# Optimization experiments

Hardware: AMD Instinct MI355X
Metric: run time of the kernel (lower is better)

## Reference

```python
import jax, jax.numpy as jnp
import numpy as np

B, S, H = 2, 2048, 2560
NH, NKV, D = 8, 4, 256
SW = 1024
EPS = 1e-6
NEG = -1e9


def _rms(x, w=None, eps=EPS):
    y = x * jax.lax.rsqrt(jnp.mean(x * x, axis=-1, keepdims=True) + eps)
    return y * (1.0 + w) if w is not None else y


def _rope(x, cos, sin):
    # x: [B, h, S, D]; cos/sin: [1, 1, S, D] with duplicated half-frequencies
    half = x.shape[-1] // 2
    out = x * cos
    o1 = out[..., :half] - x[..., half:] * sin[..., :half]
    o2 = out[..., half:] + x[..., :half] * sin[..., half:]
    return jnp.concatenate([o1, o2], axis=-1)


def setup_inputs() -> dict:
    key = jax.random.key(0)
    ks = jax.random.split(key, 6)
    hidden_states = jax.random.normal(ks[0], (B, S, H), dtype=jnp.float32)
    Wq = jax.random.normal(ks[1], (NH * D, H), dtype=jnp.float32) * 0.02
    Wk = jax.random.normal(ks[2], (NKV * D, H), dtype=jnp.float32) * 0.02
    Wv = jax.random.normal(ks[3], (NKV * D, H), dtype=jnp.float32) * 0.02
    Wo = jax.random.normal(ks[4], (H, NH * D), dtype=jnp.float32) * 0.02
    q_norm_w = jnp.zeros((D,), dtype=jnp.float32)
    k_norm_w = jnp.zeros((D,), dtype=jnp.float32)
    # RoPE tables (standard theta=10000, duplicated halves as in torch ref)
    pos = jnp.arange(S, dtype=jnp.float32)
    inv = 1.0 / (10000.0 ** (jnp.arange(0, D, 2, dtype=jnp.float32) / D))
    freqs = pos[:, None] * inv[None, :]            # [S, D/2]
    emb = jnp.concatenate([freqs, freqs], axis=-1)  # [S, D]
    cos = jnp.cos(emb)[None, None]                 # [1,1,S,D]
    sin = jnp.sin(emb)[None, None]
    # causal + sliding-window additive mask (allowed: i-SW < j <= i)
    i = jnp.arange(S)[:, None]
    j = jnp.arange(S)[None, :]
    allowed = (j <= i) & (j > i - SW)
    attention_mask = jnp.where(allowed, 0.0, NEG).astype(jnp.float32)[None, None]
    return {"hidden_states": hidden_states, "attention_mask": attention_mask,
            "cos": cos, "sin": sin, "Wq": Wq, "Wk": Wk, "Wv": Wv, "Wo": Wo,
            "q_norm_w": q_norm_w, "k_norm_w": k_norm_w}


def reference(hidden_states, attention_mask, cos, sin, Wq, Wk, Wv, Wo, q_norm_w, k_norm_w):
    b, s, _ = hidden_states.shape
    xq = (hidden_states @ Wq.T).reshape(b, s, NH, D).transpose(0, 2, 1, 3)  # [B,NH,S,D]
    xq = _rms(xq, q_norm_w)
    xk = (hidden_states @ Wk.T).reshape(b, s, NKV, D)
    xv = (hidden_states @ Wv.T).reshape(b, s, NKV, D)
    xk = _rms(xk, k_norm_w)
    xv = _rms(xv)  # parameterless rms_norm on v
    xk = xk.transpose(0, 2, 1, 3)  # [B,NKV,S,D]
    xv = xv.transpose(0, 2, 1, 3)
    xq = _rope(xq, cos, sin)
    xk = _rope(xk, cos, sin)
    # expand_kv path: S >= sliding_window and NH != NKV -> repeat_interleave
    g = NH // NKV
    xk = jnp.repeat(xk, g, axis=1)
    xv = jnp.repeat(xv, g, axis=1)
    # scale=1.0 in original (no 1/sqrt(d))
    scores = jnp.einsum('bhqd,bhkd->bhqk', xq, xk) + attention_mask
    attn = jax.nn.softmax(scores, axis=-1)
    out = jnp.einsum('bhqk,bhkd->bhqd', attn, xv)
    out = out.transpose(0, 2, 1, 3).reshape(b, s, NH * D)
    return out @ Wo.T
```

## Files before the change

kernel.cpp:

```cpp
#include <hip/hip_runtime.h>

#define B_   2
#define S_   2048
#define H_   2560
#define NH_  8
#define NKV_ 4
#define D_   256
#define SW_  1024

#define QKV_LD 4096

typedef __attribute__((ext_vector_type(8))) short    short8;
typedef __attribute__((ext_vector_type(8))) _Float16 half8;
typedef __attribute__((ext_vector_type(4))) _Float16 half4;
typedef __attribute__((ext_vector_type(4))) float    floatx4;
typedef __attribute__((ext_vector_type(2))) float    floatx2;

typedef unsigned int __attribute__((address_space(1))) as1_uint;
typedef unsigned int __attribute__((address_space(3))) as3_uint;

static __device__ __forceinline__ void async16(const void* g, void* l) {
    __builtin_amdgcn_global_load_lds((const as1_uint*)g, (as3_uint*)l, 16, 0, 0);
}

__global__ __launch_bounds__(256) void conv_all(
    const float* __restrict__ s0, const float* __restrict__ s1,
    const float* __restrict__ s2, const float* __restrict__ s3,
    const float* __restrict__ s4,
    _Float16* __restrict__ d0, _Float16* __restrict__ d1,
    _Float16* __restrict__ d2, _Float16* __restrict__ d3,
    _Float16* __restrict__ d4)
{
    const float* src; _Float16* dst; int n4;
    switch (blockIdx.y) {
        case 0:  src = s0; dst = d0; n4 = 4096 * 2560 / 4; break;
        case 1:  src = s1; dst = d1; n4 = 2048 * 2560 / 4; break;
        case 2:  src = s2; dst = d2; n4 = 1024 * 2560 / 4; break;
        case 3:  src = s3; dst = d3; n4 = 1024 * 2560 / 4; break;
        default: src = s4; dst = d4; n4 = 2560 * 2048 / 4; break;
    }
    for (int i = blockIdx.x * 256 + threadIdx.x; i < n4; i += gridDim.x * 256) {
        floatx4 v = *(const floatx4*)(src + (size_t)i * 4);
        half4 h = { (_Float16)v.x, (_Float16)v.y, (_Float16)v.z, (_Float16)v.w };
        *(half4*)(dst + (size_t)i * 4) = h;
    }
}

template <int C_FP32>
__global__ __launch_bounds__(512, 2) void gemm256(
    const _Float16* __restrict__ A,
    const _Float16* __restrict__ Bm,
    void* __restrict__ Cv,
    int M, int N, int K, int NBX)
{
    (void)M;
    __shared__ __align__(16) _Float16 As[2][256 * 64];
    __shared__ __align__(16) _Float16 Bs[2][256 * 64];

    const int tid  = threadIdx.x;
    const int lane = tid & 63, w = tid >> 6;
    const int wr = w >> 2, wc = w & 3;
    const int quad = lane >> 4, l16 = lane & 15;

    const int nwg = gridDim.x, cpx = nwg >> 3;
    const int swz = (blockIdx.x & 7) * cpx + (blockIdx.x >> 3);
    const int mBase = (swz / NBX) * 256, nBase = (swz % NBX) * 256;

    const int NT = K >> 6;

    const int stRow = w * 8 + (lane >> 3);
    const int stCol = (((lane & 7) ^ (lane >> 3)) << 3);
    const int rdsw  = (l16 & 7) << 3;

    const _Float16* Ag = A  + (size_t)mBase * K;
    const _Float16* Bg = Bm + (size_t)nBase * K;

    floatx4 acc[8][4];
    const floatx4 fz = {0.f, 0.f, 0.f, 0.f};
#pragma unroll
    for (int i = 0; i < 8; ++i)
#pragma unroll
        for (int j = 0; j < 4; ++j) acc[i][j] = fz;

    auto stA = [&](int tt, int h, _Float16* dst) {
#pragma unroll
        for (int r = 0; r < 2; ++r) {
            const int rb = h * 128 + r * 64;
            async16(Ag + (size_t)(rb + stRow) * K + tt * 64 + stCol,
                    dst + (size_t)(rb + w * 8) * 64);
        }
    };
    auto stB = [&](int tt, int h, _Float16* dst) {
#pragma unroll
        for (int r = 0; r < 2; ++r) {
            const int rb = h * 128 + r * 64;
            async16(Bg + (size_t)(rb + stRow) * K + tt * 64 + stCol,
                    dst + (size_t)(rb + w * 8) * 64);
        }
    };

    stA(0, 0, &As[0][0]); stA(0, 1, &As[0][0]);
    stB(0, 0, &Bs[0][0]); stB(0, 1, &Bs[0][0]);
    if (NT > 1) { stB(1, 0, &Bs[1][0]); stB(1, 1, &Bs[1][0]); }
    asm volatile("s_waitcnt vmcnt(4)" ::: "memory");
    __builtin_amdgcn_s_barrier();

    auto tile = [&](int t, _Float16* Ab, _Float16* Bb, _Float16* Ao) {
        half8 bf[4][2], af[2][2];
#pragma unroll
        for (int c = 0; c < 4; ++c) {
            const int brow = wc * 64 + c * 16 + l16;
#pragma unroll
            for (int s = 0; s < 2; ++s)
                bf[c][s] = *(const half8*)&Bb[(size_t)brow * 64 + ((s * 32 + quad * 8) ^ rdsw)];
        }
#pragma unroll
        for (int r = 0; r < 2; ++r) {
            const int arow = wr * 128 + r * 16 + l16;
#pragma unroll
            for (int s = 0; s < 2; ++s)
                af[r][s] = *(const half8*)&Ab[(size_t)arow * 64 + ((s * 32 + quad * 8) ^ rdsw)];
        }
        if (t + 1 < NT) stA(t + 1, 0, Ao);
        asm volatile("s_waitcnt lgkmcnt(8)");
        __builtin_amdgcn_s_barrier();
        asm volatile("s_waitcnt lgkmcnt(0)");
        __builtin_amdgcn_s_setprio(1);
#pragma unroll
        for (int s = 0; s < 2; ++s)
#pragma unroll
            for (int c = 0; c < 4; ++c) {
                acc[0][c] = __builtin_amdgcn_mfma_f32_16x16x32_f16(af[0][s], bf[c][s], acc[0][c], 0, 0, 0);
                acc[1][c] = __builtin_amdgcn_mfma_f32_16x16x32_f16(af[1][s], bf[c][s], acc[1][c], 0, 0, 0);
            }
        __builtin_amdgcn_s_setprio(0);
        __builtin_amdgcn_s_barrier();
#pragma unroll
        for (int p = 1; p < 4; ++p) {
#pragma unroll
            for (int r = 0; r < 2; ++r) {
                const int arow = wr * 128 + (2 * p + r) * 16 + l16;
#pragma unroll
                for (int s = 0; s < 2; ++s)
                    af[r][s] = *(const half8*)&Ab[(size_t)arow * 64 + ((s * 32 + quad * 8) ^ rdsw)];
            }
            if (p == 1)      { if (t + 1 < NT) stA(t + 1, 1, Ao); }
            else if (p == 2) { if (t + 2 < NT) stB(t + 2, 0, Bb); }
            else             { if (t + 2 < NT) stB(t + 2, 1, Bb); }
            __builtin_amdgcn_s_barrier();
            asm volatile("s_waitcnt lgkmcnt(0)");
            __builtin_amdgcn_s_setprio(1);
#pragma unroll
            for (int s = 0; s < 2; ++s)
#pragma unroll
                for (int c = 0; c < 4; ++c) {
                    acc[2 * p][c]     = __builtin_amdgcn_mfma_f32_16x16x32_f16(af[0][s], bf[c][s], acc[2 * p][c], 0, 0, 0);
                    acc[2 * p + 1][c] = __builtin_amdgcn_mfma_f32_16x16x32_f16(af[1][s], bf[c][s], acc[2 * p + 1][c], 0, 0, 0);
                }
            __builtin_amdgcn_s_setprio(0);
            if (p == 3) {
                if (t < NT - 2) asm volatile("s_waitcnt vmcnt(4)" ::: "memory");
                else            asm volatile("s_waitcnt vmcnt(0)" ::: "memory");
            }
            __builtin_amdgcn_s_barrier();
        }
    };

    for (int t = 0; t < NT; t += 2) {
        tile(t,     &As[0][0], &Bs[0][0], &As[1][0]);
        tile(t + 1, &As[1][0], &Bs[1][0], &As[0][0]);
    }

#pragma unroll
    for (int fr = 0; fr < 8; ++fr) {
        const int row0 = mBase + wr * 128 + fr * 16 + quad * 4;
#pragma unroll
        for (int c = 0; c < 4; ++c) {
            const int col = nBase + wc * 64 + c * 16 + l16;
#pragma unroll
            for (int r = 0; r < 4; ++r) {
                const size_t idx = (size_t)(row0 + r) * N + col;
                if (C_FP32) ((float*)Cv)[idx] = acc[fr][c][r];
                else        ((_Float16*)Cv)[idx] = (_Float16)acc[fr][c][r];
            }
        }
    }
}

__global__ __launch_bounds__(256) void rmsrope_inplace(
    _Float16* __restrict__ qkv,
    const float* __restrict__ cosT,
    const float* __restrict__ sinT,
    const float* __restrict__ qw,
    const float* __restrict__ kw)
{
    const int t = blockIdx.x;
    const int s = t & (S_ - 1);
    const int tid = threadIdx.x, lane = tid & 63, w = tid >> 6;
    _Float16* row = qkv + (size_t)t * QKV_LD;
    const int d0 = lane * 2, d1 = 128 + lane * 2;

    floatx2 c0 = *(const floatx2*)(cosT + (size_t)s * D_ + d0);
    floatx2 c1 = *(const floatx2*)(cosT + (size_t)s * D_ + d1);
    floatx2 s0 = *(const floatx2*)(sinT + (size_t)s * D_ + d0);
    floatx2 s1 = *(const floatx2*)(sinT + (size_t)s * D_ + d1);
    floatx2 qw0 = *(const floatx2*)(qw + d0), qw1 = *(const floatx2*)(qw + d1);
    floatx2 kw0 = *(const floatx2*)(kw + d0), kw1 = *(const floatx2*)(kw + d1);

#pragma unroll
    for (int p = 0; p < 4; ++p) {
        const int v = w + p * 4;
        _Float16* x = row + v * D_;
        float x0a = (float)x[d0], x0b = (float)x[d0 + 1];
        float x1a = (float)x[d1], x1b = (float)x[d1 + 1];
        float ss = x0a * x0a + x0b * x0b + x1a * x1a + x1b * x1b;
#pragma unroll
        for (int off = 32; off > 0; off >>= 1) ss += __shfl_xor(ss, off, 64);
        const float rinv = rsqrtf(ss * (1.0f / 256.0f) + 1e-6f);
        if (v < 8) {
            const float y0a = x0a * rinv * (1.f + qw0.x), y0b = x0b * rinv * (1.f + qw0.y);
            const float y1a = x1a * rinv * (1.f + qw1.x), y1b = x1b * rinv * (1.f + qw1.y);
            x[d0] = (_Float16)(y0a * c0.x - y1a * s0.x);
            x[d0 + 1] = (_Float16)(y0b * c0.y - y1b * s0.y);
            x[d1] = (_Float16)(y1a * c1.x + y0a * s1.x);
            x[d1 + 1] = (_Float16)(y1b * c1.y + y0b * s1.y);
        } else if (v < 12) {
            const float y0a = x0a * rinv * (1.f + kw0.x), y0b = x0b * rinv * (1.f + kw0.y);
            const float y1a = x1a * rinv * (1.f + kw1.x), y1b = x1b * rinv * (1.f + kw1.y);
            x[d0] = (_Float16)(y0a * c0.x - y1a * s0.x);
            x[d0 + 1] = (_Float16)(y0b * c0.y - y1b * s0.y);
            x[d1] = (_Float16)(y1a * c1.x + y0a * s1.x);
            x[d1 + 1] = (_Float16)(y1b * c1.y + y0b * s1.y);
        } else {
            x[d0] = (_Float16)(x0a * rinv);
            x[d0 + 1] = (_Float16)(x0b * rinv);
            x[d1] = (_Float16)(x1a * rinv);
            x[d1 + 1] = (_Float16)(x1b * rinv);
        }
    }
}

__global__ __launch_bounds__(256) void transpose_v(
    const _Float16* __restrict__ qkv, _Float16* __restrict__ Vt)
{
    __shared__ _Float16 tile[64][66];
    const int s0 = blockIdx.x * 64;
    const int dd0 = blockIdx.y * 64;
    const int bk = blockIdx.z;
    const int b = bk >> 2, kvh = bk & 3;
    const _Float16* src = qkv + (size_t)(b * S_) * QKV_LD + 3072 + kvh * D_;
    _Float16* dst = Vt + (size_t)bk * D_ * S_;
    const int tx = threadIdx.x & 63, ty = threadIdx.x >> 6;
    for (int r = ty; r < 64; r += 4)
        tile[r][tx] = src[(size_t)(s0 + r) * QKV_LD + dd0 + tx];
    __syncthreads();
    for (int r = ty; r < 64; r += 4)
        dst[(size_t)(dd0 + r) * S_ + s0 + tx] = tile[tx][r];
}

#define PS_STRIDE 40

__global__ __launch_bounds__(256, 2) void attn_kernel(
    const _Float16* __restrict__ qkv,
    const _Float16* __restrict__ Vt,
    _Float16* __restrict__ Oa)
{
    __shared__ __align__(16) _Float16 Ks[2][32 * 256];
    __shared__ __align__(16) _Float16 Vs[2][256 * 32];
    __shared__ __align__(16) _Float16 Ps[4][16 * PS_STRIDE];

    const int idx = blockIdx.x;
    const int swz = (idx & 7) * 64 + (idx >> 3);
    const int qt = swz & 31, h = (swz >> 5) & 7, b = swz >> 8;
    const int qb = qt * 64;
    const int kvh = h >> 1;

    const int tid = threadIdx.x, lane = tid & 63, w = tid >> 6;
    const int quad = lane >> 4, l16 = lane & 15;
    const int q0 = qb + w * 16;

    const _Float16* Qrow = qkv + ((size_t)(b * S_ + q0 + l16)) * QKV_LD + h * D_;
    half8 qf[8];
#pragma unroll
    for (int kst = 0; kst < 8; ++kst)
        qf[kst] = *(const half8*)(Qrow + kst * 32 + quad * 8);

    floatx4 o[16];
    const floatx4 fzero = {0.f, 0.f, 0.f, 0.f};
#pragma unroll
    for (int dt = 0; dt < 16; ++dt) o[dt] = fzero;
    float mrow[4] = {-50000.f, -50000.f, -50000.f, -50000.f};
    float lrow[4] = {0.f, 0.f, 0.f, 0.f};

    const _Float16* Kbase  = qkv + (size_t)(b * S_) * QKV_LD + 2048 + kvh * D_;
    const _Float16* Vtbase = Vt + (size_t)(b * NKV_ + kvh) * D_ * S_;
    const int kb_start = (qb >= SW_) ? qb - SW_ : 0;
    const int kb_end = qb + 32;

    auto stage = [&](int kb, int bufi) {
#pragma unroll
        for (int p = 0; p < 4; ++p) {
            const int keyl = w * 8 + p * 2 + (lane >> 5);
            const int g = ((lane & 31) - keyl) & 31;
            async16(Kbase + (size_t)(kb + keyl) * QKV_LD + g * 8,
                    &Ks[bufi][(w * 8 + p * 2) * 256]);
        }
#pragma unroll
        for (int p = 0; p < 4; ++p) {
            const int drow = w * 64 + p * 16 + (lane >> 2);
            const int q = lane & 3;
            async16(Vtbase + (size_t)drow * S_ + kb + q * 8,
                    &Vs[bufi][(w * 64 + p * 16) * 32]);
        }
    };

    int buf = 0;
    stage(kb_start, 0);

    for (int kb = kb_start; kb <= kb_end; kb += 32) {
        __syncthreads();
        if (kb + 32 <= kb_end) stage(kb + 32, buf ^ 1);

        if ((kb <= q0 + 15) && (kb + 31 >= q0 - (SW_ - 1))) {
            floatx4 sacc[2];
            sacc[0] = fzero; sacc[1] = fzero;
            __builtin_amdgcn_s_setprio(1);
#pragma unroll
            for (int jt = 0; jt < 2; ++jt) {
                const int keyl = jt * 16 + l16;
#pragma unroll
                for (int kst = 0; kst < 8; ++kst) {
                    const int crot = (kst * 4 + quad + keyl) & 31;
                    half8 kf = *(const half8*)&Ks[buf][keyl * 256 + crot * 8];
                    sacc[jt] = __builtin_amdgcn_mfma_f32_16x16x32_f16(qf[kst], kf, sacc[jt], 0, 0, 0);
                }
            }
            __builtin_amdgcn_s_setprio(0);

            const int qq0 = q0 + quad * 4;
            float sval[2][4], tmax[4];
#pragma unroll
            for (int r = 0; r < 4; ++r) tmax[r] = -1e30f;
#pragma unroll
            for (int jt = 0; jt < 2; ++jt) {
                const int kg = kb + jt * 16 + l16;
#pragma unroll
                for (int r = 0; r < 4; ++r) {
                    const int qg = qq0 + r;
                    const bool ok = (unsigned)(qg - kg) < (unsigned)SW_;
                    const float vv = ok ? sacc[jt][r] : -1e30f;
                    sval[jt][r] = vv;
                    tmax[r] = fmaxf(tmax[r], vv);
                }
            }
            float alpha[4];
            bool need = false;
#pragma unroll
            for (int r = 0; r < 4; ++r) {
                float t = tmax[r];
#pragma unroll
                for (int off = 1; off < 16; off <<= 1)
                    t = fmaxf(t, __shfl_xor(t, off, 64));
                const float mold = mrow[r];
                const float mnew = (t > mold + 8.f) ? t : mold;
                alpha[r] = __expf(mold - mnew);
                need |= (mnew != mold);
                mrow[r] = mnew;
                lrow[r] *= alpha[r];
            }
            if (__any(need)) {
#pragma unroll
                for (int dt = 0; dt < 16; ++dt)
#pragma unroll
                    for (int r = 0; r < 4; ++r) o[dt][r] *= alpha[r];
            }
            float rsum[4] = {0.f, 0.f, 0.f, 0.f};
#pragma unroll
            for (int jt = 0; jt < 2; ++jt)
#pragma unroll
                for (int r = 0; r < 4; ++r) {
                    const float pv = __expf(sval[jt][r] - mrow[r]);
                    rsum[r] += pv;
                    Ps[w][(quad * 4 + r) * PS_STRIDE + jt * 16 + l16] = (_Float16)pv;
                }
#pragma unroll
            for (int r = 0; r < 4; ++r) {
#pragma unroll
                for (int off = 1; off < 16; off <<= 1)
                    rsum[r] += __shfl_xor(rsum[r], off, 64);
                lrow[r] += rsum[r];
            }

            half8 pa = *(const half8*)&Ps[w][l16 * PS_STRIDE + quad * 8];
            __builtin_amdgcn_s_setprio(1);
#pragma unroll
            for (int dt = 0; dt < 16; ++dt) {
                half8 vf = *(const half8*)&Vs[buf][(dt * 16 + l16) * 32 + quad * 8];
                o[dt] = __builtin_amdgcn_mfma_f32_16x16x32_f16(pa, vf, o[dt], 0, 0, 0);
            }
            __builtin_amdgcn_s_setprio(0);
        }
        buf ^= 1;
    }

    const int qrow = q0 + quad * 4;
#pragma unroll
    for (int r = 0; r < 4; ++r) {
        const float inv = (lrow[r] > 0.f) ? (1.0f / lrow[r]) : 0.f;
        _Float16* orow = Oa + ((size_t)(b * S_ + qrow + r)) * (NH_ * D_) + h * D_;
#pragma unroll
        for (int dt = 0; dt < 16; ++dt)
            orow[dt * 16 + l16] = (_Float16)(o[dt][r] * inv);
    }
}

extern "C" void kernel_launch(void* const* d_in, const int* in_sizes, int n_in,
                              void* d_out, int out_size, void* d_ws, size_t ws_size,
                              hipStream_t stream)
{
    (void)in_sizes; (void)n_in; (void)out_size; (void)ws_size;
    const float* hid  = (const float*)d_in[0];
    const float* cosT = (const float*)d_in[2];
    const float* sinT = (const float*)d_in[3];
    const float* Wq   = (const float*)d_in[4];
    const float* Wk   = (const float*)d_in[5];
    const float* Wv   = (const float*)d_in[6];
    const float* Wo   = (const float*)d_in[7];
    const float* qw   = (const float*)d_in[8];
    const float* kw   = (const float*)d_in[9];
    float* out = (float*)d_out;

    char* ws = (char*)d_ws;
    _Float16* qkv  = (_Float16*)(ws);
    _Float16* attn = (_Float16*)(ws + 33554432ull);
    _Float16* hidH = (_Float16*)(ws + 50331648ull);
    _Float16* wQKV = (_Float16*)(ws + 71303168ull);
    _Float16* woH  = (_Float16*)(ws + 92274688ull);
    _Float16* Vt   = (_Float16*)(ws + 102760448ull);

    conv_all<<<dim3(512, 5), 256, 0, stream>>>(
        hid, Wq, Wk, Wv, Wo,
        hidH, wQKV, wQKV + (size_t)2048 * 2560, wQKV + (size_t)3072 * 2560, woH);

    gemm256<0><<<dim3(256), 512, 0, stream>>>(hidH, wQKV, qkv, 4096, 4096, 2560, 16);
    rmsrope_inplace<<<4096, 256, 0, stream>>>(qkv, cosT, sinT, qw, kw);
    transpose_v<<<dim3(32, 4, 8), 256, 0, stream>>>(qkv, Vt);
    attn_kernel<<<dim3(512), 256, 0, stream>>>(qkv, Vt, attn);
    gemm256<1><<<dim3(160), 512, 0, stream>>>(attn, woH, out, 4096, 2560, 2048, 10);
}
```

Baseline: 405.1 us.

## Split attention work across wave pairs by key half and head-dim half

Doubles the attention block to 8 waves. Each pair of waves shares 16 query rows: in QK^T each wave handles 16 of the 32 keys, and in PV each handles half of the 256-wide head dimension. The two halves exchange row maxima and final row sums through shared memory, which lets the kernel hold half the output accumulators per wave and fits more waves per CU. The cost is two extra block barriers per key tile, and the per-wave skip of tiles outside the sliding window is dropped, so those tiles are now fully masked but still computed.

```diff
diff --git a/kernel.cpp b/kernel.cpp
--- a/kernel.cpp
+++ b/kernel.cpp
@@ -260,7 +260,7 @@
 
 #define PS_STRIDE 40
 
-__global__ __launch_bounds__(256, 2) void attn_kernel(
+__global__ __launch_bounds__(512, 2) void attn_kernel(
     const _Float16* __restrict__ qkv,
     const _Float16* __restrict__ Vt,
     _Float16* __restrict__ Oa)
@@ -268,6 +268,7 @@
     __shared__ __align__(16) _Float16 Ks[2][32 * 256];
     __shared__ __align__(16) _Float16 Vs[2][256 * 32];
     __shared__ __align__(16) _Float16 Ps[4][16 * PS_STRIDE];
+    __shared__ float mlx[4][2][16];
 
     const int idx = blockIdx.x;
     const int swz = (idx & 7) * 64 + (idx >> 3);
@@ -276,8 +277,9 @@
     const int kvh = h >> 1;
 
     const int tid = threadIdx.x, lane = tid & 63, w = tid >> 6;
+    const int qsub = w >> 1, kh = w & 1;
     const int quad = lane >> 4, l16 = lane & 15;
-    const int q0 = qb + w * 16;
+    const int q0 = qb + qsub * 16;
 
     const _Float16* Qrow = qkv + ((size_t)(b * S_ + q0 + l16)) * QKV_LD + h * D_;
     half8 qf[8];
@@ -285,10 +287,10 @@
     for (int kst = 0; kst < 8; ++kst)
         qf[kst] = *(const half8*)(Qrow + kst * 32 + quad * 8);
 
-    floatx4 o[16];
+    floatx4 o[8];
     const floatx4 fzero = {0.f, 0.f, 0.f, 0.f};
 #pragma unroll
-    for (int dt = 0; dt < 16; ++dt) o[dt] = fzero;
+    for (int i = 0; i < 8; ++i) o[i] = fzero;
     float mrow[4] = {-50000.f, -50000.f, -50000.f, -50000.f};
     float lrow[4] = {0.f, 0.f, 0.f, 0.f};
 
@@ -299,18 +301,18 @@
 
     auto stage = [&](int kb, int bufi) {
 #pragma unroll
-        for (int p = 0; p < 4; ++p) {
-            const int keyl = w * 8 + p * 2 + (lane >> 5);
+        for (int p = 0; p < 2; ++p) {
+            const int keyl = w * 4 + p * 2 + (lane >> 5);
             const int g = ((lane & 31) - keyl) & 31;
             async16(Kbase + (size_t)(kb + keyl) * QKV_LD + g * 8,
-                    &Ks[bufi][(w * 8 + p * 2) * 256]);
-        }
-#pragma unroll
-        for (int p = 0; p < 4; ++p) {
-            const int drow = w * 64 + p * 16 + (lane >> 2);
+                    &Ks[bufi][(w * 4 + p * 2) * 256]);
+        }
+#pragma unroll
+        for (int p = 0; p < 2; ++p) {
+            const int drow = w * 32 + p * 16 + (lane >> 2);
             const int q = lane & 3;
             async16(Vtbase + (size_t)drow * S_ + kb + q * 8,
-                    &Vs[bufi][(w * 64 + p * 16) * 32]);
+                    &Vs[bufi][(w * 32 + p * 16) * 32]);
         }
     };
 
@@ -321,96 +323,98 @@
         __syncthreads();
         if (kb + 32 <= kb_end) stage(kb + 32, buf ^ 1);
 
-        if ((kb <= q0 + 15) && (kb + 31 >= q0 - (SW_ - 1))) {
-            floatx4 sacc[2];
-            sacc[0] = fzero; sacc[1] = fzero;
-            __builtin_amdgcn_s_setprio(1);
-#pragma unroll
-            for (int jt = 0; jt < 2; ++jt) {
-                const int keyl = jt * 16 + l16;
-#pragma unroll
-                for (int kst = 0; kst < 8; ++kst) {
-                    const int crot = (kst * 4 + quad + keyl) & 31;
-                    half8 kf = *(const half8*)&Ks[buf][keyl * 256 + crot * 8];
-                    sacc[jt] = __builtin_amdgcn_mfma_f32_16x16x32_f16(qf[kst], kf, sacc[jt], 0, 0, 0);
-                }
-            }
-            __builtin_amdgcn_s_setprio(0);
-
-            const int qq0 = q0 + quad * 4;
-            float sval[2][4], tmax[4];
-#pragma unroll
-            for (int r = 0; r < 4; ++r) tmax[r] = -1e30f;
-#pragma unroll
-            for (int jt = 0; jt < 2; ++jt) {
-                const int kg = kb + jt * 16 + l16;
-#pragma unroll
-                for (int r = 0; r < 4; ++r) {
-                    const int qg = qq0 + r;
-                    const bool ok = (unsigned)(qg - kg) < (unsigned)SW_;
-                    const float vv = ok ? sacc[jt][r] : -1e30f;
-                    sval[jt][r] = vv;
-                    tmax[r] = fmaxf(tmax[r], vv);
-                }
-            }
-            float alpha[4];
-            bool need = false;
-#pragma unroll
-            for (int r = 0; r < 4; ++r) {
-                float t = tmax[r];
-#pragma unroll
-                for (int off = 1; off < 16; off <<= 1)
-                    t = fmaxf(t, __shfl_xor(t, off, 64));
-                const float mold = mrow[r];
-                const float mnew = (t > mold + 8.f) ? t : mold;
-                alpha[r] = __expf(mold - mnew);
-                need |= (mnew != mold);
-                mrow[r] = mnew;
-                lrow[r] *= alpha[r];
-            }
-            if (__any(need)) {
-#pragma unroll
-                for (int dt = 0; dt < 16; ++dt)
-#pragma unroll
-                    for (int r = 0; r < 4; ++r) o[dt][r] *= alpha[r];
-            }
-            float rsum[4] = {0.f, 0.f, 0.f, 0.f};
-#pragma unroll
-            for (int jt = 0; jt < 2; ++jt)
-#pragma unroll
-                for (int r = 0; r < 4; ++r) {
-                    const float pv = __expf(sval[jt][r] - mrow[r]);
-                    rsum[r] += pv;
-                    Ps[w][(quad * 4 + r) * PS_STRIDE + jt * 16 + l16] = (_Float16)pv;
-                }
-#pragma unroll
-            for (int r = 0; r < 4; ++r) {
-#pragma unroll
-                for (int off = 1; off < 16; off <<= 1)
-                    rsum[r] += __shfl_xor(rsum[r], off, 64);
-                lrow[r] += rsum[r];
-            }
-
-            half8 pa = *(const half8*)&Ps[w][l16 * PS_STRIDE + quad * 8];
-            __builtin_amdgcn_s_setprio(1);
-#pragma unroll
-            for (int dt = 0; dt < 16; ++dt) {
-                half8 vf = *(const half8*)&Vs[buf][(dt * 16 + l16) * 32 + quad * 8];
-                o[dt] = __builtin_amdgcn_mfma_f32_16x16x32_f16(pa, vf, o[dt], 0, 0, 0);
-            }
-            __builtin_amdgcn_s_setprio(0);
-        }
+        floatx4 sacc = fzero;
+        const int keyl = kh * 16 + l16;
+        __builtin_amdgcn_s_setprio(1);
+#pragma unroll
+        for (int kst = 0; kst < 8; ++kst) {
+            const int crot = (kst * 4 + quad + keyl) & 31;
+            half8 kf = *(const half8*)&Ks[buf][keyl * 256 + crot * 8];
+            sacc = __builtin_amdgcn_mfma_f32_16x16x32_f16(qf[kst], kf, sacc, 0, 0, 0);
+        }
+        __builtin_amdgcn_s_setprio(0);
+
+        const int qq0 = q0 + quad * 4;
+        const int kg = kb + keyl;
+        float sval[4], hm[4];
+#pragma unroll
+        for (int r = 0; r < 4; ++r) {
+            const int qg = qq0 + r;
+            const bool ok = (unsigned)(qg - kg) < (unsigned)SW_;
+            sval[r] = ok ? sacc[r] : -1e30f;
+            float t = sval[r];
+#pragma unroll
+            for (int off = 1; off < 16; off <<= 1)
+                t = fmaxf(t, __shfl_xor(t, off, 64));
+            hm[r] = t;
+        }
+        if (l16 == 0) {
+#pragma unroll
+            for (int r = 0; r < 4; ++r) mlx[qsub][kh][quad * 4 + r] = hm[r];
+        }
+        asm volatile("s_waitcnt lgkmcnt(0)\n\ts_barrier" ::: "memory");
+
+        float alpha[4];
+        bool need = false;
+#pragma unroll
+        for (int r = 0; r < 4; ++r) {
+            const float pm = fmaxf(mlx[qsub][0][quad * 4 + r], mlx[qsub][1][quad * 4 + r]);
+            const float mold = mrow[r];
+            const float mnew = (pm > mold + 8.f) ? pm : mold;
+            alpha[r] = __expf(mold - mnew);
+            need |= (mnew != mold);
+            mrow[r] = mnew;
+            lrow[r] *= alpha[r];
+        }
+        if (__any(need)) {
+#pragma unroll
+            for (int i = 0; i < 8; ++i)
+#pragma unroll
+                for (int r = 0; r < 4; ++r) o[i][r] *= alpha[r];
+        }
+        float rsum[4];
+#pragma unroll
+        for (int r = 0; r < 4; ++r) {
+            const float pv = __expf(sval[r] - mrow[r]);
+            rsum[r] = pv;
+            Ps[qsub][(quad * 4 + r) * PS_STRIDE + kh * 16 + l16] = (_Float16)pv;
+        }
+#pragma unroll
+        for (int r = 0; r < 4; ++r) {
+#pragma unroll
+            for (int off = 1; off < 16; off <<= 1)
+                rsum[r] += __shfl_xor(rsum[r], off, 64);
+            lrow[r] += rsum[r];
+        }
+        asm volatile("s_waitcnt lgkmcnt(0)\n\ts_barrier" ::: "memory");
+
+        half8 pa = *(const half8*)&Ps[qsub][l16 * PS_STRIDE + quad * 8];
+        __builtin_amdgcn_s_setprio(1);
+#pragma unroll
+        for (int i = 0; i < 8; ++i) {
+            const int dt = kh * 8 + i;
+            half8 vf = *(const half8*)&Vs[buf][(dt * 16 + l16) * 32 + quad * 8];
+            o[i] = __builtin_amdgcn_mfma_f32_16x16x32_f16(pa, vf, o[i], 0, 0, 0);
+        }
+        __builtin_amdgcn_s_setprio(0);
         buf ^= 1;
     }
 
-    const int qrow = q0 + quad * 4;
+    __syncthreads();
+    if (l16 == 0) {
+#pragma unroll
+        for (int r = 0; r < 4; ++r) mlx[qsub][kh][quad * 4 + r] = lrow[r];
+    }
+    __syncthreads();
 #pragma unroll
     for (int r = 0; r < 4; ++r) {
-        const float inv = (lrow[r] > 0.f) ? (1.0f / lrow[r]) : 0.f;
-        _Float16* orow = Oa + ((size_t)(b * S_ + qrow + r)) * (NH_ * D_) + h * D_;
-#pragma unroll
-        for (int dt = 0; dt < 16; ++dt)
-            orow[dt * 16 + l16] = (_Float16)(o[dt][r] * inv);
+        const float lt = mlx[qsub][0][quad * 4 + r] + mlx[qsub][1][quad * 4 + r];
+        const float inv = (lt > 0.f) ? (1.0f / lt) : 0.f;
+        const int qrow = q0 + quad * 4 + r;
+        _Float16* orow = Oa + ((size_t)(b * S_ + qrow)) * (NH_ * D_) + h * D_;
+#pragma unroll
+        for (int i = 0; i < 8; ++i)
+            orow[(kh * 8 + i) * 16 + l16] = (_Float16)(o[i][r] * inv);
     }
 }
 
@@ -445,6 +449,6 @@
     gemm256<0><<<dim3(256), 512, 0, stream>>>(hidH, wQKV, qkv, 4096, 4096, 2560, 16);
     rmsrope_inplace<<<4096, 256, 0, stream>>>(qkv, cosT, sinT, qw, kw);
     transpose_v<<<dim3(32, 4, 8), 256, 0, stream>>>(qkv, Vt);
-    attn_kernel<<<dim3(512), 256, 0, stream>>>(qkv, Vt, attn);
+    attn_kernel<<<dim3(512), 512, 0, stream>>>(qkv, Vt, attn);
     gemm256<1><<<dim3(160), 512, 0, stream>>>(attn, woH, out, 4096, 2560, 2048, 10);
 }
```

Result: slower. 457.7 us (+13.0%).
